# Kernel tuning notes

Hardware: AMD Instinct MI355X
Metric: run time of the kernel (lower is better)

Reference implementation:

```python
import jax, jax.numpy as jnp
import numpy as np

CODE_STD = 0.01
EPS = 1e-12


def setup_inputs() -> dict:
    key = jax.random.key(0)
    kx, kc = jax.random.split(key)
    N, D, K = 8192, 512, 16384
    x = jax.random.normal(kx, (N, D), dtype=jnp.float32)
    codebook = CODE_STD * jax.random.normal(kc, (K, D), dtype=jnp.float32)
    return {"x": x, "codebook": codebook}


def reference(x, codebook):
    # normalize_embedding: L2-normalize each embedding vector
    emb = x / jnp.maximum(jnp.linalg.norm(x, axis=-1, keepdims=True), EPS)
    # [N, D] @ [D, K] -> [N, K] similarities
    sims = emb @ codebook.T
    best = jnp.argmax(sims, axis=1)            # [N] int32
    return codebook[best]                       # [N, D] gathered codes
```

## Files before the change

### kernel.cpp

```cpp
#include <hip/hip_runtime.h>
#include <hip/hip_bf16.h>
#include <stdint.h>


typedef float f32x4 __attribute__((ext_vector_type(4)));
typedef int int4v __attribute__((ext_vector_type(4)));
typedef int int8v __attribute__((ext_vector_type(8)));

#define M_ROWS 8192
#define DIM 512
#define K_CODES 16384
#define BM 128
#define BN 128
#define BK 128
#define NSPLIT 64
#define NT ((K_CODES / NSPLIT) / BN)
#define NEG_INF (-3.402823466e+38f)
#define MARGIN 3.2f
#define CB_SCALE 64.0f
#define N4X (M_ROWS * DIM / 4)
#define N4C (K_CODES * DIM / 4)

typedef __attribute__((address_space(1))) uint32_t as1_u32;
typedef __attribute__((address_space(3))) uint32_t as3_u32;

__device__ __forceinline__ void gll16(const void* g, void* l) {
  __builtin_amdgcn_global_load_lds((const as1_u32*)(uintptr_t)g,
                                   (as3_u32*)(uintptr_t)l, 16, 0, 0);
}

__device__ __forceinline__ void stage_tile_fp8(const uint8_t* __restrict__ g_base,
                                               uint8_t* lds_tile, int tid) {
#pragma unroll
  for (int r = 0; r < 4; ++r) {
    const int s = r * 256 + tid;
    const int row = s >> 3;
    const int kc = (s & 7) ^ (row & 7);
    const uint8_t* g = g_base + (size_t)row * DIM + (kc << 4);
    uint8_t* l = lds_tile + ((size_t)(r * 256 + (tid & 192)) << 4);
    gll16((const void*)g, (void*)l);
  }
}

__global__ void cvt_fp8(const float* __restrict__ x, const float* __restrict__ cb,
                        uint8_t* __restrict__ xd, uint8_t* __restrict__ cd) {
  int i = blockIdx.x * 256 + threadIdx.x;
  const float* src;
  uint8_t* dst;
  float sc;
  if (i < N4X) {
    src = x; dst = xd; sc = 1.0f;
  } else {
    src = cb; dst = cd; sc = CB_SCALE; i -= N4X;
    if (i >= N4C) return;
  }
  const float4 v = reinterpret_cast<const float4*>(src)[i];
  int w = 0;
  w = __builtin_amdgcn_cvt_pk_fp8_f32(v.x * sc, v.y * sc, w, false);
  w = __builtin_amdgcn_cvt_pk_fp8_f32(v.z * sc, v.w * sc, w, true);
  reinterpret_cast<int*>(dst)[i] = w;
}

__global__ __launch_bounds__(256, 2) void vq_argmax(
    const uint8_t* __restrict__ xq, const uint8_t* __restrict__ cq,
    float* __restrict__ pv, int* __restrict__ pi) {
  __shared__ __align__(16) uint8_t sxa[BM * BK];
  __shared__ __align__(16) uint8_t scb[BN * BK];
  __shared__ float rv1[2][BM], rv2[2][BM];
  __shared__ int ri1[2][BM], ri2[2][BM];

  const int tid = threadIdx.x;
  const int w = tid >> 6, lane = tid & 63;
  const int wm = w & 1, wn = w >> 1;
  const int l15 = lane & 15, quad = lane >> 4;
  const int row0 = blockIdx.x * BM;
  const int split = blockIdx.y;
  const int n_base = split * (K_CODES / NSPLIT);
  const int sw = l15 & 7;

  float bv1[4][4], bv2[4][4];
  int bi1[4][4], bi2[4][4];
#pragma unroll
  for (int i = 0; i < 4; ++i)
#pragma unroll
    for (int r = 0; r < 4; ++r) {
      bv1[i][r] = NEG_INF; bv2[i][r] = NEG_INF;
      bi1[i][r] = 0x7fffffff; bi2[i][r] = 0x7fffffff;
    }

#pragma unroll 1
  for (int nt = 0; nt < NT; ++nt) {
    const int n0 = n_base + nt * BN;
    f32x4 acc[4][4];
#pragma unroll
    for (int i = 0; i < 4; ++i)
#pragma unroll
      for (int j = 0; j < 4; ++j) acc[i][j] = (f32x4){0.f, 0.f, 0.f, 0.f};

#pragma unroll 1
    for (int ks = 0; ks < DIM / BK; ++ks) {
      const int k0 = ks * BK;
      stage_tile_fp8(xq + (size_t)row0 * DIM + k0, sxa, tid);
      stage_tile_fp8(cq + (size_t)n0 * DIM + k0, scb, tid);
      __syncthreads();

      int8v A[4], B[4];
#pragma unroll
      for (int i = 0; i < 4; ++i) {
        const int ra = (wm * 64 + i * 16 + l15) * BK;
        const int rb = (wn * 64 + i * 16 + l15) * BK;
        int4v alo = *(const int4v*)&sxa[ra + ((((quad << 1) | 0) ^ sw) << 4)];
        int4v ahi = *(const int4v*)&sxa[ra + ((((quad << 1) | 1) ^ sw) << 4)];
        int4v blo = *(const int4v*)&scb[rb + ((((quad << 1) | 0) ^ sw) << 4)];
        int4v bhi = *(const int4v*)&scb[rb + ((((quad << 1) | 1) ^ sw) << 4)];
        A[i] = __builtin_shufflevector(alo, ahi, 0, 1, 2, 3, 4, 5, 6, 7);
        B[i] = __builtin_shufflevector(blo, bhi, 0, 1, 2, 3, 4, 5, 6, 7);
      }
#pragma unroll
      for (int i = 0; i < 4; ++i)
#pragma unroll
        for (int j = 0; j < 4; ++j)
          acc[i][j] = __builtin_amdgcn_mfma_scale_f32_16x16x128_f8f6f4(
              A[i], B[j], acc[i][j], 0 , 0 ,
              0, 0x7F7F7F7F ,
              0, 0x7F7F7F7F );
      __syncthreads();
    }

#pragma unroll
    for (int i = 0; i < 4; ++i)
#pragma unroll
      for (int r = 0; r < 4; ++r)
#pragma unroll
        for (int j = 0; j < 4; ++j) {
          float s = acc[i][j][r];
          int c = n0 + wn * 64 + j * 16 + l15;
          if (s > bv1[i][r]) {
            bv2[i][r] = bv1[i][r]; bi2[i][r] = bi1[i][r];
            bv1[i][r] = s; bi1[i][r] = c;
          } else if (s > bv2[i][r]) {
            bv2[i][r] = s; bi2[i][r] = c;
          }
        }
  }

#pragma unroll
  for (int i = 0; i < 4; ++i)
#pragma unroll
    for (int r = 0; r < 4; ++r) {
      float a1 = bv1[i][r], a2 = bv2[i][r];
      int x1 = bi1[i][r], x2 = bi2[i][r];
#pragma unroll
      for (int d = 1; d < 16; d <<= 1) {
        float b1 = __shfl_xor(a1, d), b2 = __shfl_xor(a2, d);
        int y1 = __shfl_xor(x1, d), y2 = __shfl_xor(x2, d);
        bool bw = (b1 > a1) || (b1 == a1 && y1 < x1);
        float w1 = bw ? b1 : a1;  int wi = bw ? y1 : x1;
        float l1 = bw ? a1 : b1;  int li = bw ? x1 : y1;
        float s2 = bw ? b2 : a2;  int si = bw ? y2 : x2;
        bool t = (s2 > l1) || (s2 == l1 && si < li);
        a1 = w1; x1 = wi;
        a2 = t ? s2 : l1; x2 = t ? si : li;
      }
      bv1[i][r] = a1; bi1[i][r] = x1; bv2[i][r] = a2; bi2[i][r] = x2;
    }

  if (l15 == 0) {
#pragma unroll
    for (int i = 0; i < 4; ++i)
#pragma unroll
      for (int r = 0; r < 4; ++r) {
        const int rl = wm * 64 + i * 16 + quad * 4 + r;
        rv1[wn][rl] = bv1[i][r]; ri1[wn][rl] = bi1[i][r];
        rv2[wn][rl] = bv2[i][r]; ri2[wn][rl] = bi2[i][r];
      }
  }
  __syncthreads();
  if (tid < BM) {
    float a1 = rv1[0][tid], a2 = rv2[0][tid];
    int x1 = ri1[0][tid], x2 = ri2[0][tid];
    float b1 = rv1[1][tid], b2 = rv2[1][tid];
    int y1 = ri1[1][tid], y2 = ri2[1][tid];
    bool bw = (b1 > a1) || (b1 == a1 && y1 < x1);
    float w1 = bw ? b1 : a1;  int wi = bw ? y1 : x1;
    float l1 = bw ? a1 : b1;  int li = bw ? x1 : y1;
    float s2 = bw ? b2 : a2;  int si = bw ? y2 : x2;
    bool t = (s2 > l1) || (s2 == l1 && si < li);
    float m2 = t ? s2 : l1;  int mi2 = t ? si : li;
    const size_t o = (size_t)(row0 + tid) * (NSPLIT * 2) + split * 2;
    pv[o] = w1; pi[o] = wi;
    pv[o + 1] = m2; pi[o + 1] = mi2;
  }
}

__device__ double dot64(const float* __restrict__ a, const float* __restrict__ b) {
  double s0 = 0, s1 = 0, s2 = 0, s3 = 0;
#pragma unroll 4
  for (int t = 0; t < DIM; t += 4) {
    const float4 u = *(const float4*)(a + t);
    const float4 v = *(const float4*)(b + t);
    s0 += (double)u.x * v.x; s1 += (double)u.y * v.y;
    s2 += (double)u.z * v.z; s3 += (double)u.w * v.w;
  }
  return (s0 + s1) + (s2 + s3);
}

__global__ void recheck_gather(const float* __restrict__ pv, const int* __restrict__ pi,
                               const float* __restrict__ x, const float* __restrict__ cb,
                               float* __restrict__ out) {
  const int row = blockIdx.x;
  const int lane = threadIdx.x;
  const size_t base = (size_t)row * (NSPLIT * 2);
  float v0 = pv[base + lane];      int c0 = pi[base + lane];
  float v1 = pv[base + 64 + lane]; int c1 = pi[base + 64 + lane];

  bool b = (v1 > v0) || (v1 == v0 && c1 < c0);
  float m1 = b ? v1 : v0; int mi1 = b ? c1 : c0;
#pragma unroll
  for (int d = 1; d < 64; d <<= 1) {
    float ov = __shfl_xor(m1, d);
    int oi = __shfl_xor(mi1, d);
    if (ov > m1 || (ov == m1 && oi < mi1)) { m1 = ov; mi1 = oi; }
  }

  const bool f0 = (v0 >= m1 - MARGIN);
  const bool f1 = (v1 >= m1 - MARGIN);
  const int nf = __popcll(__ballot(f0)) + __popcll(__ballot(f1));
  int winner;
  if (nf == 1) {
    winner = mi1;
  } else {
    const float* xr = x + (size_t)row * DIM;
    double e = -1.0e300; int ei = 0x7fffffff;
    if (f0) { e = dot64(xr, cb + (size_t)c0 * DIM); ei = c0; }
    if (f1) {
      double e2 = dot64(xr, cb + (size_t)c1 * DIM);
      if (e2 > e || (e2 == e && c1 < ei)) { e = e2; ei = c1; }
    }
#pragma unroll
    for (int d = 1; d < 64; d <<= 1) {
      double oe = __shfl_xor(e, d);
      int oi = __shfl_xor(ei, d);
      if (oe > e || (oe == e && oi < ei)) { e = oe; ei = oi; }
    }
    winner = ei;
  }

  const float4* src = (const float4*)(cb + (size_t)winner * DIM);
  float4* dst = (float4*)(out + (size_t)row * DIM);
  dst[lane] = src[lane];
  dst[lane + 64] = src[lane + 64];
}

extern "C" void kernel_launch(void* const* d_in, const int* in_sizes, int n_in,
                              void* d_out, int out_size, void* d_ws, size_t ws_size,
                              hipStream_t stream) {
  const float* x = (const float*)d_in[0];
  const float* cb = (const float*)d_in[1];
  float* out = (float*)d_out;

  uint8_t* xq = (uint8_t*)d_ws;
  uint8_t* cq = xq + (size_t)M_ROWS * DIM;
  float* pv = (float*)(cq + (size_t)K_CODES * DIM);
  int* pi = (int*)(pv + (size_t)M_ROWS * NSPLIT * 2);

  cvt_fp8<<<(N4X + N4C + 255) / 256, 256, 0, stream>>>(x, cb, xq, cq);
  vq_argmax<<<dim3(M_ROWS / BM, NSPLIT), 256, 0, stream>>>(xq, cq, pv, pi);
  recheck_gather<<<M_ROWS, 64, 0, stream>>>(pv, pi, x, cb, out);
}
```

Measured before the change: 321.7 us.

## Load MFMA operands directly from global memory, dropping LDS staging

Removes the LDS tiles and async global-to-LDS staging with barriers. Each wave now loads its fp8 A and B fragments straight from global memory into registers, covering 128 codes per wave across two 64-code sub-tiles. This drops the barriers and LDS traffic, but loses cross-wave data sharing and leaves uncoalesced 32-byte per-lane global loads with no prefetch. Performance now depends on L1/L2 hit rates.

Result: slower. 671.0 us (+108.6%).

```diff
diff --git a/kernel.cpp b/kernel.cpp
--- a/kernel.cpp
+++ b/kernel.cpp
@@ -11,36 +11,13 @@
 #define DIM 512
 #define K_CODES 16384
 #define BM 128
-#define BN 128
-#define BK 128
 #define NSPLIT 64
-#define NT ((K_CODES / NSPLIT) / BN)
+#define CPS (K_CODES / NSPLIT)
 #define NEG_INF (-3.402823466e+38f)
 #define MARGIN 3.2f
 #define CB_SCALE 64.0f
 #define N4X (M_ROWS * DIM / 4)
 #define N4C (K_CODES * DIM / 4)
-
-typedef __attribute__((address_space(1))) uint32_t as1_u32;
-typedef __attribute__((address_space(3))) uint32_t as3_u32;
-
-__device__ __forceinline__ void gll16(const void* g, void* l) {
-  __builtin_amdgcn_global_load_lds((const as1_u32*)(uintptr_t)g,
-                                   (as3_u32*)(uintptr_t)l, 16, 0, 0);
-}
-
-__device__ __forceinline__ void stage_tile_fp8(const uint8_t* __restrict__ g_base,
-                                               uint8_t* lds_tile, int tid) {
-#pragma unroll
-  for (int r = 0; r < 4; ++r) {
-    const int s = r * 256 + tid;
-    const int row = s >> 3;
-    const int kc = (s & 7) ^ (row & 7);
-    const uint8_t* g = g_base + (size_t)row * DIM + (kc << 4);
-    uint8_t* l = lds_tile + ((size_t)(r * 256 + (tid & 192)) << 4);
-    gll16((const void*)g, (void*)l);
-  }
-}
 
 __global__ void cvt_fp8(const float* __restrict__ x, const float* __restrict__ cb,
                         uint8_t* __restrict__ xd, uint8_t* __restrict__ cd) {
@@ -61,11 +38,15 @@
   reinterpret_cast<int*>(dst)[i] = w;
 }
 
+__device__ __forceinline__ int8v load32(const uint8_t* p) {
+  int4v lo = *(const int4v*)p;
+  int4v hi = *(const int4v*)(p + 16);
+  return __builtin_shufflevector(lo, hi, 0, 1, 2, 3, 4, 5, 6, 7);
+}
+
 __global__ __launch_bounds__(256, 2) void vq_argmax(
     const uint8_t* __restrict__ xq, const uint8_t* __restrict__ cq,
     float* __restrict__ pv, int* __restrict__ pi) {
-  __shared__ __align__(16) uint8_t sxa[BM * BK];
-  __shared__ __align__(16) uint8_t scb[BN * BK];
   __shared__ float rv1[2][BM], rv2[2][BM];
   __shared__ int ri1[2][BM], ri2[2][BM];
 
@@ -75,8 +56,10 @@
   const int l15 = lane & 15, quad = lane >> 4;
   const int row0 = blockIdx.x * BM;
   const int split = blockIdx.y;
-  const int n_base = split * (K_CODES / NSPLIT);
-  const int sw = l15 & 7;
+  const int cbase = split * CPS + wn * 128;
+
+  const uint8_t* abase = xq + (size_t)(row0 + wm * 64 + l15) * DIM + (quad << 5);
+  const uint8_t* bbase = cq + (size_t)(cbase + l15) * DIM + (quad << 5);
 
   float bv1[4][4], bv2[4][4];
   int bi1[4][4], bi2[4][4];
@@ -88,43 +71,30 @@
       bi1[i][r] = 0x7fffffff; bi2[i][r] = 0x7fffffff;
     }
 
-#pragma unroll 1
-  for (int nt = 0; nt < NT; ++nt) {
-    const int n0 = n_base + nt * BN;
+#pragma unroll
+  for (int js = 0; js < 2; ++js) {
     f32x4 acc[4][4];
 #pragma unroll
     for (int i = 0; i < 4; ++i)
 #pragma unroll
       for (int j = 0; j < 4; ++j) acc[i][j] = (f32x4){0.f, 0.f, 0.f, 0.f};
 
-#pragma unroll 1
-    for (int ks = 0; ks < DIM / BK; ++ks) {
-      const int k0 = ks * BK;
-      stage_tile_fp8(xq + (size_t)row0 * DIM + k0, sxa, tid);
-      stage_tile_fp8(cq + (size_t)n0 * DIM + k0, scb, tid);
-      __syncthreads();
-
+#pragma unroll
+    for (int ks = 0; ks < 4; ++ks) {
       int8v A[4], B[4];
 #pragma unroll
-      for (int i = 0; i < 4; ++i) {
-        const int ra = (wm * 64 + i * 16 + l15) * BK;
-        const int rb = (wn * 64 + i * 16 + l15) * BK;
-        int4v alo = *(const int4v*)&sxa[ra + ((((quad << 1) | 0) ^ sw) << 4)];
-        int4v ahi = *(const int4v*)&sxa[ra + ((((quad << 1) | 1) ^ sw) << 4)];
-        int4v blo = *(const int4v*)&scb[rb + ((((quad << 1) | 0) ^ sw) << 4)];
-        int4v bhi = *(const int4v*)&scb[rb + ((((quad << 1) | 1) ^ sw) << 4)];
-        A[i] = __builtin_shufflevector(alo, ahi, 0, 1, 2, 3, 4, 5, 6, 7);
-        B[i] = __builtin_shufflevector(blo, bhi, 0, 1, 2, 3, 4, 5, 6, 7);
-      }
+      for (int i = 0; i < 4; ++i)
+        A[i] = load32(abase + (size_t)(i * 16) * DIM + ks * 128);
+#pragma unroll
+      for (int j = 0; j < 4; ++j)
+        B[j] = load32(bbase + (size_t)(js * 64 + j * 16) * DIM + ks * 128);
 #pragma unroll
       for (int i = 0; i < 4; ++i)
 #pragma unroll
         for (int j = 0; j < 4; ++j)
           acc[i][j] = __builtin_amdgcn_mfma_scale_f32_16x16x128_f8f6f4(
               A[i], B[j], acc[i][j], 0 , 0 ,
-              0, 0x7F7F7F7F ,
-              0, 0x7F7F7F7F );
-      __syncthreads();
+              0, 0x7F7F7F7F , 0, 0x7F7F7F7F );
     }
 
 #pragma unroll
@@ -134,7 +104,7 @@
 #pragma unroll
         for (int j = 0; j < 4; ++j) {
           float s = acc[i][j][r];
-          int c = n0 + wn * 64 + j * 16 + l15;
+          int c = cbase + js * 64 + j * 16 + l15;
           if (s > bv1[i][r]) {
             bv2[i][r] = bv1[i][r]; bi2[i][r] = bi1[i][r];
             bv1[i][r] = s; bi1[i][r] = c;
```
